# Optimization experiments

Measured on AMD Instinct MI355X. Metric: run time of the kernel, lower is better.

The kernel has to match this reference:

```python
import jax, jax.numpy as jnp
import numpy as np

FEAT = 1024
SUPPORT = 512
N = 4096


def setup_inputs() -> dict:
    key = jax.random.key(0)
    k1, k2, k3, k4, k5, k6 = jax.random.split(key, 6)
    s = 1.0 / np.sqrt(FEAT)
    f = jax.random.normal(k1, (N, FEAT), dtype=jnp.float32)
    G = jax.random.normal(k2, (SUPPORT, FEAT), dtype=jnp.float32)
    # PyTorch LSTMCell params: weight_ih [4*hidden, input], weight_hh [4*hidden, hidden]
    W_ih = jax.random.uniform(k3, (4 * FEAT, 2 * FEAT), minval=-s, maxval=s, dtype=jnp.float32)
    W_hh = jax.random.uniform(k4, (4 * FEAT, FEAT), minval=-s, maxval=s, dtype=jnp.float32)
    b_ih = jax.random.uniform(k5, (4 * FEAT,), minval=-s, maxval=s, dtype=jnp.float32)
    b_hh = jax.random.uniform(k6, (4 * FEAT,), minval=-s, maxval=s, dtype=jnp.float32)
    return {"f": f, "G": G, "W_ih": W_ih, "W_hh": W_hh, "b_ih": b_ih, "b_hh": b_hh, "n_ways": 20}


def _lstm_cell(x, h, c, W_ih, W_hh, b_ih, b_hh):
    # gates ordered i, f, g, o as in torch.nn.LSTMCell
    gates = x @ W_ih.T + b_ih + h @ W_hh.T + b_hh  # [N, 4*FEAT]
    i, fg, g, o = jnp.split(gates, 4, axis=1)
    i = jax.nn.sigmoid(i)
    fg = jax.nn.sigmoid(fg)
    g = jnp.tanh(g)
    o = jax.nn.sigmoid(o)
    c_new = fg * c + i * g
    h_new = o * jnp.tanh(c_new)
    return h_new, c_new


def reference(f, G, W_ih, W_hh, b_ih, b_hh, n_ways):
    h = f
    c = jnp.zeros_like(f)  # c_0 expanded, zeros (non-learned Variable)
    for _ in range(n_ways):
        logit_a = h @ G.T                      # [N, M]
        a = jax.nn.softmax(logit_a, axis=0)    # softmax over dim 0, as in original
        r = a @ G                              # [N, FEAT]
        x = jnp.concatenate((f, r), axis=1)    # [N, 2*FEAT]
        h, c = _lstm_cell(x, h, c, W_ih, W_hh, b_ih, b_hh)
        h = h + f
    return h
```

## Files before the change

### kernel.cpp

```cpp
#include <hip/hip_runtime.h>
#include <math.h>

#define NB    4096
#define FEAT  1024
#define MSUP  512
#define G4    4096
#define NWAYS 20

typedef _Float16 f16;
typedef f16 f16x8 __attribute__((ext_vector_type(8)));
typedef f16 f16x4 __attribute__((ext_vector_type(4)));
typedef float f32x4 __attribute__((ext_vector_type(4)));
typedef unsigned int u32;
#define GLOBAL_AS __attribute__((address_space(1)))
#define LDS_AS    __attribute__((address_space(3)))

__device__ __forceinline__ void load_lds16(const void* g, void* l) {
    __builtin_amdgcn_global_load_lds((const GLOBAL_AS u32*)g, (LDS_AS u32*)l, 16, 0, 0);
}

template<int BM, int BN, int WROWS, int WCOLS, bool OUTF16, bool HASBIAS>
__global__ __launch_bounds__(256) void mfma_nt(
    void* __restrict__ Cv, int ldc,
    const f16* __restrict__ A1, int lda1, const f16* __restrict__ B1, int ldb1, int K1,
    const f16* __restrict__ A2, int lda2, const f16* __restrict__ B2, int ldb2, int K2,
    const f16* __restrict__ A3, int lda3, const f16* __restrict__ B3, int ldb3, int K3,
    const float* __restrict__ bias1, const float* __restrict__ bias2)
{
    constexpr int BK = 32;
    constexpr int WM = BM / WROWS, WN = BN / WCOLS;
    constexpr int FM = WM / 16,   FN = WN / 16;
    __shared__ f16 As[BM][BK];
    __shared__ f16 Bs[BN][BK];
    const int tid  = threadIdx.x;
    const int lane = tid & 63;
    const int wrow = (tid >> 6) % WROWS, wcol = (tid >> 6) / WROWS;
    const int bm = blockIdx.y * BM, bn = blockIdx.x * BN;
    const int lr = lane & 15, lq = lane >> 4;

    f32x4 acc[FM][FN] = {};

    #pragma unroll
    for (int pass = 0; pass < 3; ++pass) {
        const f16* A = pass == 0 ? A1 : (pass == 1 ? A2 : A3);
        const f16* B = pass == 0 ? B1 : (pass == 1 ? B2 : B3);
        const int lda = pass == 0 ? lda1 : (pass == 1 ? lda2 : lda3);
        const int ldb = pass == 0 ? ldb1 : (pass == 1 ? ldb2 : ldb3);
        const int K   = pass == 0 ? K1  : (pass == 1 ? K2  : K3);
        if (!A) break;
        #pragma unroll 1
        for (int k0 = 0; k0 < K; k0 += BK) {
            __syncthreads();
            #pragma unroll
            for (int t = 0; t < (BM * 4) / 256; ++t) {
                int c = t * 256 + tid;
                load_lds16(A + (size_t)(bm + (c >> 2)) * lda + k0 + (c & 3) * 8,
                           &As[0][0] + ((size_t)t * 256 + (tid & 192)) * 8);
            }
            #pragma unroll
            for (int t = 0; t < (BN * 4) / 256; ++t) {
                int c = t * 256 + tid;
                load_lds16(B + (size_t)(bn + (c >> 2)) * ldb + k0 + (c & 3) * 8,
                           &Bs[0][0] + ((size_t)t * 256 + (tid & 192)) * 8);
            }
            __syncthreads();
            f16x8 af[FM], bf[FN];
            #pragma unroll
            for (int i = 0; i < FM; ++i)
                af[i] = *(const f16x8*)&As[wrow * WM + i * 16 + lr][lq * 8];
            #pragma unroll
            for (int j = 0; j < FN; ++j)
                bf[j] = *(const f16x8*)&Bs[wcol * WN + j * 16 + lr][lq * 8];
            #pragma unroll
            for (int i = 0; i < FM; ++i)
                #pragma unroll
                for (int j = 0; j < FN; ++j)
                    acc[i][j] = __builtin_amdgcn_mfma_f32_16x16x32_f16(af[i], bf[j], acc[i][j], 0, 0, 0);
        }
    }

    #pragma unroll
    for (int i = 0; i < FM; ++i) {
        #pragma unroll
        for (int j = 0; j < FN; ++j) {
            const int col  = bn + wcol * WN + j * 16 + lr;
            const int row0 = bm + wrow * WM + i * 16 + lq * 4;
            float badd = 0.f;
            if (HASBIAS) badd = bias1[col] + bias2[col];
            #pragma unroll
            for (int r = 0; r < 4; ++r) {
                size_t off = (size_t)(row0 + r) * ldc + col;
                float v = acc[i][j][r] + badd;
                if (OUTF16) ((f16*)Cv)[off] = (f16)v;
                else        ((float*)Cv)[off] = v;
            }
        }
    }
}

__global__ __launch_bounds__(256) void softmax_rows_kernel(
    const float* __restrict__ X, f16* __restrict__ Y)
{
    const int row = blockIdx.x;
    const float* x = X + (size_t)row * NB;
    f16* y = Y + (size_t)row * NB;
    const int tid = threadIdx.x;
    float v[16];
    float mx = -1e30f;
    #pragma unroll
    for (int i = 0; i < 16; ++i) { v[i] = x[tid + (i << 8)]; mx = fmaxf(mx, v[i]); }
    #pragma unroll
    for (int off = 32; off > 0; off >>= 1) mx = fmaxf(mx, __shfl_down(mx, off));
    __shared__ float sm[4];
    if ((tid & 63) == 0) sm[tid >> 6] = mx;
    __syncthreads();
    mx = fmaxf(fmaxf(sm[0], sm[1]), fmaxf(sm[2], sm[3]));
    float s = 0.f;
    #pragma unroll
    for (int i = 0; i < 16; ++i) { v[i] = __expf(v[i] - mx); s += v[i]; }
    #pragma unroll
    for (int off = 32; off > 0; off >>= 1) s += __shfl_down(s, off);
    __shared__ float ss[4];
    if ((tid & 63) == 0) ss[tid >> 6] = s;
    __syncthreads();
    s = ss[0] + ss[1] + ss[2] + ss[3];
    const float inv = 1.f / s;
    #pragma unroll
    for (int i = 0; i < 16; ++i) y[tid + (i << 8)] = (f16)(v[i] * inv);
}

__global__ __launch_bounds__(256) void transpose_f16_kernel(
    const f16* __restrict__ in, f16* __restrict__ out, int R, int C)
{
    __shared__ f16 t[64][65];
    const int r0 = blockIdx.y * 64, c0 = blockIdx.x * 64;
    const int lr = threadIdx.x & 63, lw = threadIdx.x >> 6;
    #pragma unroll
    for (int i = 0; i < 16; ++i) {
        int rr = lw * 16 + i;
        t[rr][lr] = in[(size_t)(r0 + rr) * C + c0 + lr];
    }
    __syncthreads();
    #pragma unroll
    for (int i = 0; i < 16; ++i) {
        int cc = lw * 16 + i;
        out[(size_t)(c0 + cc) * R + r0 + lr] = t[lr][cc];
    }
}

__global__ __launch_bounds__(256) void cvt_f16_kernel(
    const float* __restrict__ in, f16* __restrict__ out, int n)
{
    int idx = (blockIdx.x * 256 + threadIdx.x) * 4;
    if (idx < n) {
        float4 v = *(const float4*)(in + idx);
        f16x4 o = {(f16)v.x, (f16)v.y, (f16)v.z, (f16)v.w};
        *(f16x4*)(out + idx) = o;
    }
}

__global__ __launch_bounds__(256) void split_hilo_kernel(
    const float* __restrict__ in, f16* __restrict__ hi, f16* __restrict__ lo, int n)
{
    int idx = (blockIdx.x * 256 + threadIdx.x) * 4;
    if (idx < n) {
        float4 v = *(const float4*)(in + idx);
        f16x4 h = {(f16)v.x, (f16)v.y, (f16)v.z, (f16)v.w};
        f16x4 l = {(f16)(v.x - (float)h.x), (f16)(v.y - (float)h.y),
                   (f16)(v.z - (float)h.z), (f16)(v.w - (float)h.w)};
        *(f16x4*)(hi + idx) = h;
        *(f16x4*)(lo + idx) = l;
    }
}

__global__ __launch_bounds__(256) void lstm_cell_kernel(
    const f16* __restrict__ gates, const f16* __restrict__ pre,
    const float* __restrict__ f,
    float* __restrict__ c, float* __restrict__ h, f16* __restrict__ h_h, int first)
{
    const int idx = (blockIdx.x * 256 + threadIdx.x) * 4;
    const int n = idx >> 10, k = idx & 1023;
    const f16* g = gates + (size_t)n * G4 + k;
    const f16* p = pre   + (size_t)n * G4 + k;
    f16x4 gi = *(const f16x4*)(g);
    f16x4 gf = *(const f16x4*)(g + 1024);
    f16x4 gg = *(const f16x4*)(g + 2048);
    f16x4 go = *(const f16x4*)(g + 3072);
    f16x4 pi = *(const f16x4*)(p);
    f16x4 pf = *(const f16x4*)(p + 1024);
    f16x4 pg = *(const f16x4*)(p + 2048);
    f16x4 po = *(const f16x4*)(p + 3072);
    float4 cold = {0.f, 0.f, 0.f, 0.f};
    if (!first) cold = *(const float4*)(c + idx);
    float4 fv = *(const float4*)(f + idx);
    float cn[4], hn[4];
    const float co[4] = {cold.x, cold.y, cold.z, cold.w};
    const float fo[4] = {fv.x, fv.y, fv.z, fv.w};
    #pragma unroll
    for (int u = 0; u < 4; ++u) {
        float ig = (float)gi[u] + (float)pi[u];
        float fg = (float)gf[u] + (float)pf[u];
        float g_ = (float)gg[u] + (float)pg[u];
        float og = (float)go[u] + (float)po[u];
        float i_ = 1.f / (1.f + __expf(-ig));
        float f_ = 1.f / (1.f + __expf(-fg));
        float gt = tanhf(g_);
        float o_ = 1.f / (1.f + __expf(-og));
        cn[u] = i_ * gt + f_ * co[u];
        hn[u] = o_ * tanhf(cn[u]) + fo[u];
    }
    *(float4*)(c + idx) = {cn[0], cn[1], cn[2], cn[3]};
    *(float4*)(h + idx) = {hn[0], hn[1], hn[2], hn[3]};
    f16x4 hh = {(f16)hn[0], (f16)hn[1], (f16)hn[2], (f16)hn[3]};
    *(f16x4*)(h_h + idx) = hh;
}

extern "C" void kernel_launch(void* const* d_in, const int* in_sizes, int n_in,
                              void* d_out, int out_size, void* d_ws, size_t ws_size,
                              hipStream_t stream) {
    const float* f   = (const float*)d_in[0];
    const float* G   = (const float*)d_in[1];
    const float* Wih = (const float*)d_in[2];
    const float* Whh = (const float*)d_in[3];
    const float* bih = (const float*)d_in[4];
    const float* bhh = (const float*)d_in[5];
    float* h = (float*)d_out;

    char* W = (char*)d_ws;
    f16*   pre_h   = (f16*)(W);
    f16*   gates_h = (f16*)(W + (size_t)(32 << 20));
    float* aT      = (float*)(W + (size_t)(64 << 20));
    f16*   aTh     = (f16*)(W + (size_t)(72 << 20));
    f16*   a_h     = (f16*)(W + (size_t)(76 << 20));
    float* c       = (float*)(W + (size_t)(80 << 20));
    f16*   h_h     = (f16*)(W + (size_t)(96 << 20));
    f16*   Wih_h   = (f16*)(W + (size_t)(104 << 20));
    f16*   Whh_h   = (f16*)(W + (size_t)(120 << 20));
    float* Wr32    = (float*)(W + (size_t)(128 << 20));
    f16*   Wr_hi   = (f16*)(W + (size_t)(136 << 20));
    f16*   Wr_lo   = (f16*)(W + (size_t)(140 << 20));
    f16*   G_h     = (f16*)(W + (size_t)(144 << 20));

    const f16* NF = nullptr;
    const dim3 blk(256);

    cvt_f16_kernel<<<(NB * FEAT) / 1024, blk, 0, stream>>>(f, h_h, NB * FEAT);
    cvt_f16_kernel<<<(G4 * 2 * FEAT) / 1024, blk, 0, stream>>>(Wih, Wih_h, G4 * 2 * FEAT);
    cvt_f16_kernel<<<(G4 * FEAT) / 1024, blk, 0, stream>>>(Whh, Whh_h, G4 * FEAT);
    cvt_f16_kernel<<<(MSUP * FEAT) / 1024, blk, 0, stream>>>(G, G_h, MSUP * FEAT);

    mfma_nt<128, 128, 2, 2, true, true><<<dim3(G4 / 128, NB / 128), blk, 0, stream>>>(
        pre_h, G4,
        h_h, FEAT, Wih_h, 2 * FEAT, FEAT,
        NF, 0, NF, 0, 0,
        NF, 0, NF, 0, 0,
        bih, bhh);

    mfma_nt<128, 128, 2, 2, false, false><<<dim3(MSUP / 128, G4 / 128), blk, 0, stream>>>(
        Wr32, MSUP,
        Wih_h + FEAT, 2 * FEAT, G_h, FEAT, FEAT,
        NF, 0, NF, 0, 0,
        NF, 0, NF, 0, 0,
        nullptr, nullptr);
    split_hilo_kernel<<<(G4 * MSUP) / 1024, blk, 0, stream>>>(Wr32, Wr_hi, Wr_lo, G4 * MSUP);

    for (int it = 0; it < NWAYS; ++it) {
        mfma_nt<64, 64, 2, 2, false, false><<<dim3(NB / 64, MSUP / 64), blk, 0, stream>>>(
            aT, NB,
            G_h, FEAT, h_h, FEAT, FEAT,
            NF, 0, NF, 0, 0,
            NF, 0, NF, 0, 0,
            nullptr, nullptr);

        softmax_rows_kernel<<<MSUP, blk, 0, stream>>>(aT, aTh);

        transpose_f16_kernel<<<dim3(NB / 64, MSUP / 64), blk, 0, stream>>>(aTh, a_h, MSUP, NB);

        mfma_nt<128, 128, 2, 2, true, false><<<dim3(G4 / 128, NB / 128), blk, 0, stream>>>(
            gates_h, G4,
            a_h, MSUP, Wr_hi, MSUP, MSUP,
            a_h, MSUP, Wr_lo, MSUP, MSUP,
            h_h, FEAT, Whh_h, FEAT, FEAT,
            nullptr, nullptr);

        lstm_cell_kernel<<<(NB * FEAT) / 1024, blk, 0, stream>>>(gates_h, pre_h, f, c, h, h_h, it == 0);
    }
}
```

Baseline: 3.012 ms.

## Fuse LSTM cell into gate GEMM epilogue via interleaved gate permutation

Permutes the rows of W_ih, W_hh and the bias so that the four gates of each feature land in adjacent output columns. This lets the gate GEMM epilogue gather all four gates with lane shuffles and compute the LSTM cell in-register. The fp16 gates buffer round trip and the separate lstm_cell kernel launch go away. The cell state is stored in a tile-native layout, h ping-pongs between two fp16 buffers, and the fp32 output is written only on the last iteration. The price is more epilogue work inside the GEMM, with scattered 2-byte stores and uncoalesced pre/f reads.

After: 3.066 ms. About the same (+1.8%).

```diff
diff --git a/kernel.cpp b/kernel.cpp
--- a/kernel.cpp
+++ b/kernel.cpp
@@ -19,13 +19,21 @@
     __builtin_amdgcn_global_load_lds((const GLOBAL_AS u32*)g, (LDS_AS u32*)l, 16, 0, 0);
 }
 
-template<int BM, int BN, int WROWS, int WCOLS, bool OUTF16, bool HASBIAS>
+__device__ __forceinline__ float sigm(float x) { return 1.f / (1.f + __expf(-x)); }
+
+template<int BM, int BN, int WROWS, int WCOLS, bool OUTF16, bool HASBIAS, bool FUSECELL>
 __global__ __launch_bounds__(256) void mfma_nt(
     void* __restrict__ Cv, int ldc,
     const f16* __restrict__ A1, int lda1, const f16* __restrict__ B1, int ldb1, int K1,
     const f16* __restrict__ A2, int lda2, const f16* __restrict__ B2, int ldb2, int K2,
     const f16* __restrict__ A3, int lda3, const f16* __restrict__ B3, int ldb3, int K3,
-    const float* __restrict__ bias1, const float* __restrict__ bias2)
+    const float* __restrict__ bias,
+    const f16* __restrict__ pre,
+    const float* __restrict__ fin,
+    float* __restrict__ cbuf,
+    f16* __restrict__ hh,
+    float* __restrict__ hout,
+    int first, int writeH)
 {
     constexpr int BK = 32;
     constexpr int WM = BM / WROWS, WN = BN / WCOLS;
@@ -79,20 +87,57 @@
         }
     }
 
-    #pragma unroll
-    for (int i = 0; i < FM; ++i) {
+    if (FUSECELL) {
+        const int q  = lane & 3;
+        const int kk = (lane >> 2) & 3;
         #pragma unroll
-        for (int j = 0; j < FN; ++j) {
-            const int col  = bn + wcol * WN + j * 16 + lr;
-            const int row0 = bm + wrow * WM + i * 16 + lq * 4;
-            float badd = 0.f;
-            if (HASBIAS) badd = bias1[col] + bias2[col];
-            #pragma unroll
-            for (int r = 0; r < 4; ++r) {
-                size_t off = (size_t)(row0 + r) * ldc + col;
-                float v = acc[i][j][r] + badd;
-                if (OUTF16) ((f16*)Cv)[off] = (f16)v;
-                else        ((float*)Cv)[off] = v;
+        for (int i = 0; i < FM; ++i) {
+            #pragma unroll
+            for (int j = 0; j < FN; ++j) {
+                const int col  = bn + wcol * WN + j * 16 + lr;
+                const int row0 = bm + wrow * WM + i * 16 + lq * 4;
+                float x[4];
+                #pragma unroll
+                for (int r = 0; r < 4; ++r)
+                    x[r] = acc[i][j][r] + (float)pre[(size_t)(row0 + r) * G4 + col];
+                float g4[4];
+                #pragma unroll
+                for (int k = 0; k < 4; ++k) {
+                    int srcq = (q + k) & 3;
+                    int src  = (lane & ~3) | srcq;
+                    g4[srcq] = __shfl(x[(q - k + 4) & 3], src, 64);
+                }
+                const int row  = row0 + q;
+                const int feat = ((bn + wcol * WN + j * 16) >> 2) + kk;
+                const float i_ = sigm(g4[0]);
+                const float f_ = sigm(g4[1]);
+                const float g_ = tanhf(g4[2]);
+                const float o_ = sigm(g4[3]);
+                const size_t cid = ((size_t)(blockIdx.y * gridDim.x + blockIdx.x) * (FM * FN)
+                                    + i * FN + j) * 256 + tid;
+                float cold = first ? 0.f : cbuf[cid];
+                float cn = i_ * g_ + f_ * cold;
+                cbuf[cid] = cn;
+                float hn = o_ * tanhf(cn) + fin[(size_t)row * FEAT + feat];
+                hh[(size_t)row * FEAT + feat] = (f16)hn;
+                if (writeH) hout[(size_t)row * FEAT + feat] = hn;
+            }
+        }
+    } else {
+        #pragma unroll
+        for (int i = 0; i < FM; ++i) {
+            #pragma unroll
+            for (int j = 0; j < FN; ++j) {
+                const int col  = bn + wcol * WN + j * 16 + lr;
+                const int row0 = bm + wrow * WM + i * 16 + lq * 4;
+                float badd = HASBIAS ? bias[col] : 0.f;
+                #pragma unroll
+                for (int r = 0; r < 4; ++r) {
+                    size_t off = (size_t)(row0 + r) * ldc + col;
+                    float v = acc[i][j][r] + badd;
+                    if (OUTF16) ((f16*)Cv)[off] = (f16)v;
+                    else        ((float*)Cv)[off] = v;
+                }
             }
         }
     }
@@ -157,6 +202,24 @@
         f16x4 o = {(f16)v.x, (f16)v.y, (f16)v.z, (f16)v.w};
         *(f16x4*)(out + idx) = o;
     }
+}
+
+__global__ __launch_bounds__(256) void cvt_perm_kernel(
+    const float* __restrict__ in, f16* __restrict__ out, int ld)
+{
+    int idx = (blockIdx.x * 256 + threadIdx.x) * 4;
+    int j = idx / ld, k = idx % ld;
+    int dst = 4 * (j & 1023) + (j >> 10);
+    float4 v = *(const float4*)(in + idx);
+    f16x4 o = {(f16)v.x, (f16)v.y, (f16)v.z, (f16)v.w};
+    *(f16x4*)(out + (size_t)dst * ld + k) = o;
+}
+
+__global__ __launch_bounds__(256) void bias_perm_kernel(
+    const float* __restrict__ bih, const float* __restrict__ bhh, float* __restrict__ out)
+{
+    int j = blockIdx.x * 256 + threadIdx.x;
+    out[4 * (j & 1023) + (j >> 10)] = bih[j] + bhh[j];
 }
 
 __global__ __launch_bounds__(256) void split_hilo_kernel(
@@ -171,48 +234,6 @@
         *(f16x4*)(hi + idx) = h;
         *(f16x4*)(lo + idx) = l;
     }
-}
-
-__global__ __launch_bounds__(256) void lstm_cell_kernel(
-    const f16* __restrict__ gates, const f16* __restrict__ pre,
-    const float* __restrict__ f,
-    float* __restrict__ c, float* __restrict__ h, f16* __restrict__ h_h, int first)
-{
-    const int idx = (blockIdx.x * 256 + threadIdx.x) * 4;
-    const int n = idx >> 10, k = idx & 1023;
-    const f16* g = gates + (size_t)n * G4 + k;
-    const f16* p = pre   + (size_t)n * G4 + k;
-    f16x4 gi = *(const f16x4*)(g);
-    f16x4 gf = *(const f16x4*)(g + 1024);
-    f16x4 gg = *(const f16x4*)(g + 2048);
-    f16x4 go = *(const f16x4*)(g + 3072);
-    f16x4 pi = *(const f16x4*)(p);
-    f16x4 pf = *(const f16x4*)(p + 1024);
-    f16x4 pg = *(const f16x4*)(p + 2048);
-    f16x4 po = *(const f16x4*)(p + 3072);
-    float4 cold = {0.f, 0.f, 0.f, 0.f};
-    if (!first) cold = *(const float4*)(c + idx);
-    float4 fv = *(const float4*)(f + idx);
-    float cn[4], hn[4];
-    const float co[4] = {cold.x, cold.y, cold.z, cold.w};
-    const float fo[4] = {fv.x, fv.y, fv.z, fv.w};
-    #pragma unroll
-    for (int u = 0; u < 4; ++u) {
-        float ig = (float)gi[u] + (float)pi[u];
-        float fg = (float)gf[u] + (float)pf[u];
-        float g_ = (float)gg[u] + (float)pg[u];
-        float og = (float)go[u] + (float)po[u];
-        float i_ = 1.f / (1.f + __expf(-ig));
-        float f_ = 1.f / (1.f + __expf(-fg));
-        float gt = tanhf(g_);
-        float o_ = 1.f / (1.f + __expf(-og));
-        cn[u] = i_ * gt + f_ * co[u];
-        hn[u] = o_ * tanhf(cn[u]) + fo[u];
-    }
-    *(float4*)(c + idx) = {cn[0], cn[1], cn[2], cn[3]};
-    *(float4*)(h + idx) = {hn[0], hn[1], hn[2], hn[3]};
-    f16x4 hh = {(f16)hn[0], (f16)hn[1], (f16)hn[2], (f16)hn[3]};
-    *(f16x4*)(h_h + idx) = hh;
 }
 
 extern "C" void kernel_launch(void* const* d_in, const int* in_sizes, int n_in,
@@ -228,61 +249,61 @@
 
     char* W = (char*)d_ws;
     f16*   pre_h   = (f16*)(W);
-    f16*   gates_h = (f16*)(W + (size_t)(32 << 20));
-    float* aT      = (float*)(W + (size_t)(64 << 20));
-    f16*   aTh     = (f16*)(W + (size_t)(72 << 20));
-    f16*   a_h     = (f16*)(W + (size_t)(76 << 20));
-    float* c       = (float*)(W + (size_t)(80 << 20));
-    f16*   h_h     = (f16*)(W + (size_t)(96 << 20));
-    f16*   Wih_h   = (f16*)(W + (size_t)(104 << 20));
-    f16*   Whh_h   = (f16*)(W + (size_t)(120 << 20));
-    float* Wr32    = (float*)(W + (size_t)(128 << 20));
-    f16*   Wr_hi   = (f16*)(W + (size_t)(136 << 20));
-    f16*   Wr_lo   = (f16*)(W + (size_t)(140 << 20));
-    f16*   G_h     = (f16*)(W + (size_t)(144 << 20));
+    float* aT      = (float*)(W + (size_t)(32 << 20));
+    f16*   aTh     = (f16*)(W + (size_t)(40 << 20));
+    f16*   a_h     = (f16*)(W + (size_t)(44 << 20));
+    float* cbuf    = (float*)(W + (size_t)(48 << 20));
+    f16*   h0      = (f16*)(W + (size_t)(64 << 20));
+    f16*   hA      = (f16*)(W + (size_t)(72 << 20));
+    f16*   hB      = (f16*)(W + (size_t)(80 << 20));
+    f16*   Wih_h   = (f16*)(W + (size_t)(88 << 20));
+    f16*   Whh_h   = (f16*)(W + (size_t)(104 << 20));
+    float* Wr32    = (float*)(W + (size_t)(112 << 20));
+    f16*   Wr_hi   = (f16*)(W + (size_t)(120 << 20));
+    f16*   Wr_lo   = (f16*)(W + (size_t)(124 << 20));
+    f16*   G_h     = (f16*)(W + (size_t)(128 << 20));
+    float* bias_p  = (float*)(W + (size_t)(129 << 20));
 
     const f16* NF = nullptr;
     const dim3 blk(256);
 
-    cvt_f16_kernel<<<(NB * FEAT) / 1024, blk, 0, stream>>>(f, h_h, NB * FEAT);
-    cvt_f16_kernel<<<(G4 * 2 * FEAT) / 1024, blk, 0, stream>>>(Wih, Wih_h, G4 * 2 * FEAT);
-    cvt_f16_kernel<<<(G4 * FEAT) / 1024, blk, 0, stream>>>(Whh, Whh_h, G4 * FEAT);
+    cvt_f16_kernel<<<(NB * FEAT) / 1024, blk, 0, stream>>>(f, h0, NB * FEAT);
+    cvt_perm_kernel<<<(G4 * 2 * FEAT) / 1024, blk, 0, stream>>>(Wih, Wih_h, 2 * FEAT);
+    cvt_perm_kernel<<<(G4 * FEAT) / 1024, blk, 0, stream>>>(Whh, Whh_h, FEAT);
     cvt_f16_kernel<<<(MSUP * FEAT) / 1024, blk, 0, stream>>>(G, G_h, MSUP * FEAT);
-
-    mfma_nt<128, 128, 2, 2, true, true><<<dim3(G4 / 128, NB / 128), blk, 0, stream>>>(
+    bias_perm_kernel<<<G4 / 256, blk, 0, stream>>>(bih, bhh, bias_p);
+
+    mfma_nt<128, 128, 2, 2, true, true, false><<<dim3(G4 / 128, NB / 128), blk, 0, stream>>>(
         pre_h, G4,
-        h_h, FEAT, Wih_h, 2 * FEAT, FEAT,
-        NF, 0, NF, 0, 0,
-        NF, 0, NF, 0, 0,
-        bih, bhh);
-
-    mfma_nt<128, 128, 2, 2, false, false><<<dim3(MSUP / 128, G4 / 128), blk, 0, stream>>>(
+        h0, FEAT, Wih_h, 2 * FEAT, FEAT,
+        NF, 0, NF, 0, 0, NF, 0, NF, 0, 0,
+        bias_p, NF, nullptr, nullptr, nullptr, nullptr, 0, 0);
+
+    mfma_nt<128, 128, 2, 2, false, false, false><<<dim3(MSUP / 128, G4 / 128), blk, 0, stream>>>(
         Wr32, MSUP,
         Wih_h + FEAT, 2 * FEAT, G_h, FEAT, FEAT,
-        NF, 0, NF, 0, 0,
-        NF, 0, NF, 0, 0,
-        nullptr, nullptr);
+        NF, 0, NF, 0, 0, NF, 0, NF, 0, 0,
+        nullptr, NF, nullptr, nullptr, nullptr, nullptr, 0, 0);
     split_hilo_kernel<<<(G4 * MSUP) / 1024, blk, 0, stream>>>(Wr32, Wr_hi, Wr_lo, G4 * MSUP);
 
+    const f16* hcur = h0;
     for (int it = 0; it < NWAYS; ++it) {
-        mfma_nt<64, 64, 2, 2, false, false><<<dim3(NB / 64, MSUP / 64), blk, 0, stream>>>(
+        mfma_nt<64, 64, 2, 2, false, false, false><<<dim3(NB / 64, MSUP / 64), blk, 0, stream>>>(
             aT, NB,
-            G_h, FEAT, h_h, FEAT, FEAT,
-            NF, 0, NF, 0, 0,
-            NF, 0, NF, 0, 0,
-            nullptr, nullptr);
+            G_h, FEAT, hcur, FEAT, FEAT,
+            NF, 0, NF, 0, 0, NF, 0, NF, 0, 0,
+            nullptr, NF, nullptr, nullptr, nullptr, nullptr, 0, 0);
 
         softmax_rows_kernel<<<MSUP, blk, 0, stream>>>(aT, aTh);
-
         transpose_f16_kernel<<<dim3(NB / 64, MSUP / 64), blk, 0, stream>>>(aTh, a_h, MSUP, NB);
 
-        mfma_nt<128, 128, 2, 2, true, false><<<dim3(G4 / 128, NB / 128), blk, 0, stream>>>(
-            gates_h, G4,
+        f16* hnext = (it & 1) ? hB : hA;
+        mfma_nt<128, 128, 2, 2, false, false, true><<<dim3(G4 / 128, NB / 128), blk, 0, stream>>>(
+            nullptr, G4,
             a_h, MSUP, Wr_hi, MSUP, MSUP,
             a_h, MSUP, Wr_lo, MSUP, MSUP,
-            h_h, FEAT, Whh_h, FEAT, FEAT,
-            nullptr, nullptr);
-
-        lstm_cell_kernel<<<(NB * FEAT) / 1024, blk, 0, stream>>>(gates_h, pre_h, f, c, h, h_h, it == 0);
-    }
-}
+            hcur, FEAT, Whh_h, FEAT, FEAT,
+            nullptr, pre_h, f, cbuf, hnext, h, it == 0, it == NWAYS - 1);
+        hcur = hnext;
+    }
+}
```
